# Kernel tuning notes

Measured on AMD Instinct MI355X. Metric: run time of the kernel, lower is better.

## Reference

```python
import jax, jax.numpy as jnp
from jax import lax
import numpy as np

B = 4096
CUR_OBS = 256; HIST_C = 96; HIST_T = 25
FUT_FLAT = 256 * 10  # fut_ref_dim * fut_ref_seq_len
HID = 1024; PROJ = 512; HLAT = 64; FLAT = 64
CONV = HID // 4  # conv_hidden_dim
E = 16; TOPK = 4; NGROUP = 4; TOPKG = 2; ROUTE_SCALE = 1.0; NSHARED = 2; OUT = 23

silu = jax.nn.silu

def conv1d(x, w, b, stride):
    # x: [B, C_in, T], w: [C_out, C_in, K] (torch Conv1d layout), padding=1
    y = lax.conv_general_dilated(x, w, (stride,), [(1, 1)],
                                 dimension_numbers=('NCH', 'OIH', 'NCH'))
    return y + b[None, :, None]

def setup_inputs() -> dict:
    key = jax.random.key(0)
    ks = iter(jax.random.split(key, 64))
    def nrm(shape, s=0.02):
        return jax.random.normal(next(ks), shape, jnp.float32) * s
    d = {}
    d['cur_obs'] = jax.random.normal(next(ks), (B, CUR_OBS), jnp.float32)
    d['cur_hist_seq'] = jax.random.normal(next(ks), (B, HIST_T, HIST_C), jnp.float32)
    d['fut_ref'] = jax.random.normal(next(ks), (B, FUT_FLAT), jnp.float32)
    d['vae_noise'] = jax.random.normal(next(ks), (B, FLAT), jnp.float32)
    # history conv encoder
    d['conv1_w'] = nrm((CONV, HIST_C, 3));      d['conv1_b'] = nrm((CONV,))
    d['conv2_w'] = nrm((2 * CONV, CONV, 3));    d['conv2_b'] = nrm((2 * CONV,))
    d['conv3_w'] = nrm((4 * CONV, 2 * CONV, 3)); d['conv3_b'] = nrm((4 * CONV,))
    d['hlin1_w'] = nrm((4 * CONV, HID)); d['hlin1_b'] = nrm((HID,))
    d['hlin2_w'] = nrm((HID, HLAT));     d['hlin2_b'] = nrm((HLAT,))
    # fut-ref VAE encoder
    d['enc1_w'] = nrm((FUT_FLAT, HID)); d['enc1_b'] = nrm((HID,))
    d['enc2_w'] = nrm((HID, HID));      d['enc2_b'] = nrm((HID,))
    d['enc3_w'] = nrm((HID, 2 * FLAT)); d['enc3_b'] = nrm((2 * FLAT,))
    # input projection
    d['proj_w'] = nrm((CUR_OBS + HLAT + FLAT, PROJ)); d['proj_b'] = nrm((PROJ,))
    # router
    d['router_w'] = nrm((PROJ, E)); d['router_b'] = nrm((E,))
    # stacked fine experts (DeepseekV3MLP x E)
    d['Wg'] = nrm((E, PROJ, HID)); d['bg'] = nrm((E, HID))
    d['Wu'] = nrm((E, PROJ, HID)); d['bu'] = nrm((E, HID))
    d['Wd'] = nrm((E, HID, PROJ)); d['bd'] = nrm((E, PROJ))
    # shared experts (intermediate = HID * NSHARED)
    d['sh_g_w'] = nrm((PROJ, HID * NSHARED)); d['sh_g_b'] = nrm((HID * NSHARED,))
    d['sh_u_w'] = nrm((PROJ, HID * NSHARED)); d['sh_u_b'] = nrm((HID * NSHARED,))
    d['sh_d_w'] = nrm((HID * NSHARED, PROJ)); d['sh_d_b'] = nrm((PROJ,))
    # output mlp + head
    d['out1_w'] = nrm((PROJ, HID)); d['out1_b'] = nrm((HID,))
    d['out2_w'] = nrm((HID, HID));  d['out2_b'] = nrm((HID,))
    d['head_w'] = nrm((HID, OUT));  d['head_b'] = nrm((OUT,))
    return d


def reference(cur_obs, cur_hist_seq, fut_ref, vae_noise,
              conv1_w, conv1_b, conv2_w, conv2_b, conv3_w, conv3_b,
              hlin1_w, hlin1_b, hlin2_w, hlin2_b,
              enc1_w, enc1_b, enc2_w, enc2_b, enc3_w, enc3_b,
              proj_w, proj_b, router_w, router_b,
              Wg, bg, Wu, bu, Wd, bd,
              sh_g_w, sh_g_b, sh_u_w, sh_u_b, sh_d_w, sh_d_b,
              out1_w, out1_b, out2_w, out2_b, head_w, head_b):
    # ---- history conv encoder ----
    h = cur_hist_seq.transpose(0, 2, 1)                 # [B, C, T]
    h = silu(conv1d(h, conv1_w, conv1_b, 1))            # [B, 256, 25]
    h = silu(conv1d(h, conv2_w, conv2_b, 2))            # [B, 512, 13]
    h = silu(conv1d(h, conv3_w, conv3_b, 2))            # [B, 1024, 7]
    h = h.mean(-1)                                      # AdaptiveAvgPool1d(1)+Flatten
    hist_lat = silu(h @ hlin1_w + hlin1_b) @ hlin2_w + hlin2_b  # [B, 64]
    # ---- fut-ref VAE encoder + reparameterize ----
    e = silu(fut_ref @ enc1_w + enc1_b)
    e = silu(e @ enc2_w + enc2_b)
    mu, logvar = jnp.split(e @ enc3_w + enc3_b, 2, axis=-1)
    z = mu + jnp.exp(0.5 * logvar) * vae_noise          # [B, 64]
    # ---- projection ----
    x = jnp.concatenate([cur_obs, hist_lat, z], axis=-1) @ proj_w + proj_b  # [B, PROJ]
    # ---- DeepseekV3 top-k group router (router math in fp32) ----
    logits = x.astype(jnp.float32) @ router_w + router_b
    scores = jax.nn.sigmoid(logits)                     # [B, E]
    gs = scores.reshape(-1, NGROUP, E // NGROUP)
    group_scores = lax.top_k(gs, 2)[0].sum(-1)          # [B, NGROUP]
    gidx = lax.top_k(group_scores, TOPKG)[1]
    rows = jnp.arange(scores.shape[0])[:, None]
    gmask = jnp.zeros_like(group_scores).at[rows, gidx].set(1.0)
    smask = jnp.repeat(gmask, E // NGROUP, axis=1)      # [B, E]
    masked = jnp.where(smask > 0, scores, 0.0)
    tidx = lax.top_k(masked, TOPK)[1]                   # [B, TOPK]
    tw = jnp.take_along_axis(scores, tidx, axis=1)
    tw = tw / (tw.sum(-1, keepdims=True) + 1e-20) * ROUTE_SCALE
    # ---- MoE dispatch/combine: sparse combine weights, dense expert eval ----
    w = jnp.zeros((x.shape[0], E), jnp.float32).at[rows, tidx].add(tw)  # [B, E]
    g = jnp.einsum('bh,ehi->bei', x, Wg) + bg           # [B, E, HID]
    u = jnp.einsum('bh,ehi->bei', x, Wu) + bu
    y = jnp.einsum('bei,eih->beh', silu(g) * u, Wd) + bd  # [B, E, PROJ]
    moe_out = jnp.einsum('be,beh->bh', w, y)            # [B, PROJ]
    shared = (silu(x @ sh_g_w + sh_g_b) * (x @ sh_u_w + sh_u_b)) @ sh_d_w + sh_d_b
    h2 = moe_out + shared
    h2 = silu(h2 @ out1_w + out1_b) @ out2_w + out2_b
    return h2 @ head_w + head_b                         # actions [B, OUT]
```

## Files before the change

kernel.cpp:

```cpp
#include <hip/hip_runtime.h>
#include <hip/hip_bf16.h>


#define BATCH 4096
typedef unsigned short u16;
typedef unsigned int u32;
using bf16x8 = __attribute__((ext_vector_type(8))) __bf16;
using f32x4  = __attribute__((ext_vector_type(4))) float;

__device__ __forceinline__ float silu_f(float v) { return v / (1.f + __expf(-v)); }

__device__ __forceinline__ float b2f(u16 u) {
  union { u32 i; float f; } c; c.i = ((u32)u) << 16; return c.f;
}
__device__ __forceinline__ u16 f2b(float f) {
  union { float f; u32 i; } c; c.f = f;
  u32 r = c.i + 0x7FFFu + ((c.i >> 16) & 1u);
  return (u16)(r >> 16);
}
__device__ __forceinline__ float4 ld4(const float* p) { return *(const float4*)p; }
__device__ __forceinline__ float4 ld4(const u16* p) {
  ushort4 v = *(const ushort4*)p;
  return make_float4(b2f(v.x), b2f(v.y), b2f(v.z), b2f(v.w));
}

__device__ __forceinline__ void gll16(const u16* g, u16* l) {
  __attribute__((address_space(3))) u32* lp =
      reinterpret_cast<__attribute__((address_space(3))) u32*>(
          reinterpret_cast<uintptr_t>(l));
  __builtin_amdgcn_global_load_lds(reinterpret_cast<const u32*>(g), lp, 16, 0, 0);
}

union U8 { uint4 u; bf16x8 b; };

static constexpr size_t WT1T_B = 0;
static constexpr size_t WT2T_B = 147456;
static constexpr size_t WT3T_B = 933888;
static constexpr size_t HL1T_B = 4079616;
static constexpr size_t RA_B   = 6176768;
static constexpr size_t RB_B   = 64897024;
static constexpr size_t P_B    = 119422976;
static constexpr size_t FRH_B  = RA_B;
static constexpr size_t FRL_B  = RA_B + 20971520;
static constexpr size_t E1H_B  = RA_B + 41943040;
static constexpr size_t E1L_B  = RA_B + 50331648;
static constexpr size_t E2H_B  = RA_B;
// ... 12 lines not shown
static constexpr size_t H2_B   = RA_B + 25165824;
static constexpr size_t H2B_B  = RA_B + 33554432;
static constexpr size_t E1TH_B = RB_B;
static constexpr size_t E1TL_B = RB_B + 5242880;
static constexpr size_t E2TH_B = RB_B + 10485760;
static constexpr size_t E2TL_B = RB_B + 12582912;
static constexpr size_t PENC_B = RB_B + 14680064;
static constexpr size_t HSB_B  = RB_B;
static constexpr size_t Y2_B   = RB_B;
static constexpr size_t HB_B   = RB_B;
static constexpr size_t HI1_B  = RB_B + 8388608;
static constexpr size_t PHL2_B = RB_B + 16777216;
static constexpr size_t XCH_B  = RB_B + 16777216;
static constexpr size_t XCL_B  = RB_B + 19922944;
static constexpr size_t XH_B   = RB_B;
static constexpr size_t TM_B   = RB_B + 8388608;
static constexpr size_t STB_B  = RB_B + 8388608;
static constexpr size_t PSH_B  = RB_B + 25165824;
static constexpr size_t O1B_B  = RB_B;
static constexpr size_t O2H_B  = RB_B + 16777216;
static constexpr size_t O2L_B  = RB_B + 25165824;
static constexpr size_t PHD_B  = RB_B + 33554432;
static constexpr size_t HLAT_B = P_B;
static constexpr size_t E3P_B  = P_B + 1048576;
static constexpr size_t Z_B    = P_B + 3145728;
static constexpr size_t LOG_B  = P_B + 4194304;
static constexpr size_t TID_B  = P_B + 4456448;
static constexpr size_t TW_B   = P_B + 4521984;
static constexpr size_t POS_B  = P_B + 4587520;
static constexpr size_t CNT_B  = P_B + 4653056;
static constexpr size_t OFS_B  = P_B + 4653184;
static constexpr size_t ROWL_B = P_B + 4653312;
static constexpr size_t WL_B   = P_B + 4718848;
static constexpr size_t ZP_B   = P_B + 4784384;
static constexpr size_t PRJH_B = P_B + 4788480;
static constexpr size_t PRJL_B = P_B + 5181696;
static constexpr size_t E3TH_B = P_B + 5574912;
static constexpr size_t E3TL_B = P_B + 5837056;
static constexpr size_t HL2P_B = P_B + 6099200;
static constexpr size_t HDH_B  = P_B + 6361344;
static constexpr size_t HDL_B  = P_B + 6623488;

#define TILE_DECODE(nn_)                         \
  const int bid = blockIdx.x;                    \
  const int xcd = bid & 7;                       \
  const int tt_ = bid >> 3;                      \
  const int n0 = (tt_ % (nn_)) * 128;            \
  const int m0 = ((tt_ / (nn_)) * 8 + xcd) * 128;

__global__ void k_zero2(int* __restrict__ a, int na, int* __restrict__ b, int nb) {
  int i = blockIdx.x * 256 + threadIdx.x;
  if (i < na) a[i] = 0;
  else if (i < na + nb) b[i - na] = 0;
}
__global__ void k_zero_f4(float4* __restrict__ p, int n4) {
  int i = blockIdx.x * 256 + threadIdx.x;
  if (i < n4) p[i] = make_float4(0.f, 0.f, 0.f, 0.f);
}
__global__ void k_f32_to_bf4(const float* __restrict__ s, u16* __restrict__ d, int n4) {
  int i = blockIdx.x * 256 + threadIdx.x;
  if (i >= n4) return;
  float4 v = *(const float4*)(s + (size_t)i * 4);
  *(ushort4*)(d + (size_t)i * 4) = make_ushort4(f2b(v.x), f2b(v.y), f2b(v.z), f2b(v.w));
}
__global__ void k_split_x(const float* __restrict__ s, u16* __restrict__ dh,
                          u16* __restrict__ dl, int n4) {
  int i = blockIdx.x * 256 + threadIdx.x;
  if (i >= n4) return;
  float4 v = *(const float4*)(s + (size_t)i * 4);
  float a[4] = {v.x, v.y, v.z, v.w};
  ushort4 h, l;
  u16* hp = (u16*)&h; u16* lp = (u16*)&l;
#pragma unroll
  for (int j = 0; j < 4; ++j) {
    u16 hh = f2b(a[j]);
    hp[j] = hh;
    lp[j] = f2b(a[j] - b2f(hh));
  }
  *(ushort4*)(dh + (size_t)i * 4) = h;
  *(ushort4*)(dl + (size_t)i * 4) = l;
}
// ... 2 lines not shown
                        const float* __restrict__ bias, u16* __restrict__ Ch,
                        u16* __restrict__ Cl, int N, int n4) {
  int i = blockIdx.x * 256 + threadIdx.x;
  if (i >= n4) return;
  float4 a = *(const float4*)(P0 + (size_t)i * 4);
  float4 b = *(const float4*)(P1 + (size_t)i * 4);
  int col = (i * 4) & (N - 1);
  float r[4] = {a.x + b.x, a.y + b.y, a.z + b.z, a.w + b.w};
  ushort4 h, l;
  u16* hp = (u16*)&h; u16* lp = (u16*)&l;
#pragma unroll
  for (int j = 0; j < 4; ++j) {
    float v = r[j] + bias[col + j];
    if (ACT) v = silu_f(v);
    u16 hh = f2b(v);
    hp[j] = hh;
    lp[j] = f2b(v - b2f(hh));
  }
  *(ushort4*)(Ch + (size_t)i * 4) = h;
  *(ushort4*)(Cl + (size_t)i * 4) = l;
}
template<int ACT, int EPI>
__global__ void k_combS(const float* __restrict__ P, const float* __restrict__ bias,
                        float* __restrict__ Cf, int S, int lgNp, int Nout, int total) {
  int idx = blockIdx.x * 256 + threadIdx.x;
  if (idx >= total) return;
  int row = idx >> lgNp;
  int col = idx & ((1 << lgNp) - 1);
  if (col >= Nout) return;
  float s = 0.f;
  for (int si = 0; si < S; ++si) s += P[(size_t)si * total + idx];
  s += bias[col];
  if (ACT) s = silu_f(s);
  if (EPI == 0) Cf[(size_t)row * Nout + col] = s;
  else Cf[(size_t)row * Nout + col] += s;
}
__global__ void k_concat_split(const float* __restrict__ obs,
                               const float* __restrict__ hl,
                               const float* __restrict__ z,
                               u16* __restrict__ dh, u16* __restrict__ dl) {
  int idx = blockIdx.x * 256 + threadIdx.x;
  if (idx >= BATCH * 384) return;
  int b = idx / 384, c = idx - b * 384;
  float v;
  if (c < 256)      v = obs[(size_t)b * 256 + c];
  else if (c < 320) v = hl[(size_t)b * 64 + (c - 256)];
  else              v = z[(size_t)b * 64 + (c - 320)];
  u16 h = f2b(v);
  dh[idx] = h;
  dl[idx] = f2b(v - b2f(h));
}
__global__ void k_wt_conv3(const float* __restrict__ w1, u16* __restrict__ t1,
                           const float* __restrict__ w2, u16* __restrict__ t2,
                           const float* __restrict__ w3, u16* __restrict__ t3) {
  int idx = blockIdx.x * 256 + threadIdx.x;
  const float* w; u16* t; int CIN;
  if (idx < 73728)        { w = w1; t = t1; CIN = 96; }
  else if (idx < 466944)  { idx -= 73728;  w = w2; t = t2; CIN = 256; }
  else if (idx < 2039808) { idx -= 466944; w = w3; t = t3; CIN = 512; }
  else return;
  int Kc = CIN * 3;
  int o = idx / Kc, c = idx - o * Kc;
  int k = c / CIN, i = c - k * CIN;
  t[idx] = f2b(w[(size_t)o * Kc + i * 3 + k]);
}
__global__ __launch_bounds__(256) void k_transpose_bf(const float* __restrict__ W,
                                                      u16* __restrict__ WT,
                                                      int K, int N) {
  __shared__ float t[32][33];
  int n0 = blockIdx.x * 32, k0 = blockIdx.y * 32;
  int lx = threadIdx.x & 31, ly = threadIdx.x >> 5;
#pragma unroll
  for (int r = 0; r < 32; r += 8)
    t[ly + r][lx] = W[(size_t)(k0 + ly + r) * N + n0 + lx];
  __syncthreads();
#pragma unroll
  for (int r = 0; r < 32; r += 8)
    WT[(size_t)(n0 + ly + r) * K + k0 + lx] = f2b(t[lx][ly + r]);
}
__global__ __launch_bounds__(256) void k_transpose_bf_pad(const float* __restrict__ W,
                                                          u16* __restrict__ WT,
                                                          int K, int N) {
  __shared__ float t[32][33];
  int n0 = blockIdx.x * 32, k0 = blockIdx.y * 32;
  int lx = threadIdx.x & 31, ly = threadIdx.x >> 5;
#pragma unroll
  for (int r = 0; r < 32; r += 8)
    t[ly + r][lx] = (n0 + lx < N) ? W[(size_t)(k0 + ly + r) * N + n0 + lx] : 0.f;
  __syncthreads();
#pragma unroll
  for (int r = 0; r < 32; r += 8)
    WT[(size_t)(n0 + ly + r) * K + k0 + lx] = f2b(t[lx][ly + r]);
}
__global__ __launch_bounds__(256) void k_transpose_hilo_pad(const float* __restrict__ W,
                                                            u16* __restrict__ WTh,
                                                            u16* __restrict__ WTl,
                                                            int K, int N) {
  __shared__ float t[32][33];
  int n0 = blockIdx.x * 32, k0 = blockIdx.y * 32;
  int lx = threadIdx.x & 31, ly = threadIdx.x >> 5;
#pragma unroll
  for (int r = 0; r < 32; r += 8)
    t[ly + r][lx] = (n0 + lx < N) ? W[(size_t)(k0 + ly + r) * N + n0 + lx] : 0.f;
  __syncthreads();
#pragma unroll
  for (int r = 0; r < 32; r += 8) {
    float f = t[lx][ly + r];
    u16 h = f2b(f);
    size_t o = (size_t)(n0 + ly + r) * K + k0 + lx;
    WTh[o] = h;
    WTl[o] = f2b(f - b2f(h));
  }
}
__global__ __launch_bounds__(256) void k_transpose_bf_b(const float* __restrict__ W,
                                                        u16* __restrict__ WT,
                                                        int K, int N) {
  const size_t eo = (size_t)blockIdx.z * K * N;
  __shared__ float t[32][33];
  int n0 = blockIdx.x * 32, k0 = blockIdx.y * 32;
  int lx = threadIdx.x & 31, ly = threadIdx.x >> 5;
#pragma unroll
  for (int r = 0; r < 32; r += 8)
    t[ly + r][lx] = W[eo + (size_t)(k0 + ly + r) * N + n0 + lx];
  __syncthreads();
#pragma unroll
  for (int r = 0; r < 32; r += 8)
    WT[eo + (size_t)(n0 + ly + r) * K + k0 + lx] = f2b(t[lx][ly + r]);
}
__global__ __launch_bounds__(256) void k_transpose_hilo(const float* __restrict__ W,
                                                        u16* __restrict__ WTh,
                                                        u16* __restrict__ WTl,
                                                        int K, int N) {
  __shared__ float t[32][33];
  int n0 = blockIdx.x * 32, k0 = blockIdx.y * 32;
  int lx = threadIdx.x & 31, ly = threadIdx.x >> 5;
#pragma unroll
  for (int r = 0; r < 32; r += 8)
    t[ly + r][lx] = W[(size_t)(k0 + ly + r) * N + n0 + lx];
  __syncthreads();
#pragma unroll
  for (int r = 0; r < 32; r += 8) {
    float f = t[lx][ly + r];
    u16 h = f2b(f);
    size_t o = (size_t)(n0 + ly + r) * K + k0 + lx;
    WTh[o] = h;
    WTl[o] = f2b(f - b2f(h));
  }
}

#define PRO128 \
  const int tid = threadIdx.x; \
  const int lane = tid & 63; \
  const int wid = tid >> 6; \
  const int wr = (wid >> 1) * 64, wc = (wid & 1) * 64; \
  const int l15 = lane & 15, lsub = lane >> 4;

#define MFMA_BF16(a, b, c) __builtin_amdgcn_mfma_f32_16x16x32_bf16(a, b, c, 0, 0, 0)

template<int ACT, int EPI, int AP, int BP>
__global__ __launch_bounds__(256) void k_gg(
    const u16* __restrict__ A0, const u16* __restrict__ A1,
    const u16* __restrict__ B0, const u16* __restrict__ B1,
    const float* __restrict__ bias,
    float* __restrict__ Cf, u16* __restrict__ Ch, u16* __restrict__ Cl,
    int K, int lda, int ldb, int nn, int Nout) {
  constexpr int NT = AP + BP;
  __shared__ u16 lds[NT * 4096];
  PRO128
  TILE_DECODE(nn)
  const int r0 = wid * 32 + (lane >> 2);
// ... 608 lines not shown
#pragma unroll
        for (int ni = 0; ni < 4; ++ni)
          acc[mi][ni] = MFMA_BF16(fa[mi].b, fb[ni].b, acc[mi][ni]);
    }
    __syncthreads();
  }
  const int row4 = lsub * 4;
#pragma unroll
  for (int mi = 0; mi < 4; ++mi)
#pragma unroll
    for (int j = 0; j < 4; ++j) {
      int row = m0 + wr + mi * 16 + row4 + j;
      if (row >= ne) continue;
      int r = rowlist[base + row];
      float wl = wlist[base + row];
#pragma unroll
      for (int ni = 0; ni < 4; ++ni) {
        int col = n0 + wc + ni * 16 + l15;
        atomicAdd(&h2[(size_t)r * 512 + col], wl * (acc[mi][ni][j] + bde[col]));
      }
    }
}

template<int ACT, bool NG, typename TA>
__global__ __launch_bounds__(256) void k_gemm(const TA* __restrict__ A,
                                              const float* __restrict__ W,
                                              const float* __restrict__ bias,
                                              float* __restrict__ C,
                                              int N, int K) {
  __shared__ float As[16][64];
  __shared__ float Bs[16][64];
  const int tid = threadIdx.x;
  const int m0 = blockIdx.x * 64;
  const int n0 = blockIdx.y * 64;
  const int tr = tid >> 4, tc = tid & 15;
  const int lm = tid >> 2, lk = (tid & 3) * 4;
  const int ln = tid & 63, lkb = (tid >> 6) * 4;
  float acc[4][4] = {};
  for (int k0 = 0; k0 < K; k0 += 16) {
    float4 av = ld4(A + (size_t)(m0 + lm) * K + k0 + lk);
    As[lk + 0][lm] = av.x; As[lk + 1][lm] = av.y;
    As[lk + 2][lm] = av.z; As[lk + 3][lm] = av.w;
#pragma unroll
    for (int s = 0; s < 4; ++s) {
      int kk = lkb + s;
      float v = 0.f;
      if (!NG || (n0 + ln) < N) v = W[(size_t)(k0 + kk) * N + n0 + ln];
      Bs[kk][ln] = v;
    }
    __syncthreads();
#pragma unroll
    for (int kk = 0; kk < 16; ++kk) {
      float4 a4 = *(const float4*)&As[kk][tr * 4];
      float4 b4 = *(const float4*)&Bs[kk][tc * 4];
      float a[4] = {a4.x, a4.y, a4.z, a4.w};
      float b[4] = {b4.x, b4.y, b4.z, b4.w};
#pragma unroll
      for (int i = 0; i < 4; ++i)
#pragma unroll
        for (int j = 0; j < 4; ++j) acc[i][j] = fmaf(a[i], b[j], acc[i][j]);
    }
    __syncthreads();
  }
#pragma unroll
  for (int i = 0; i < 4; ++i) {
    int m = m0 + tr * 4 + i;
#pragma unroll
    for (int j = 0; j < 4; ++j) {
      int n = n0 + tc * 4 + j;
      if (NG && n >= N) continue;
      float v = acc[i][j] + bias[n];
      if (ACT == 1) v = silu_f(v);
      C[(size_t)m * N + n] = v;
    }
  }
}

__global__ void k_mean7(const u16* __restrict__ y3, u16* __restrict__ hb) {
  int idx = blockIdx.x * 256 + threadIdx.x;
  if (idx >= BATCH * 1024) return;
  int b = idx >> 10, o = idx & 1023;
  const u16* p = y3 + (size_t)b * 7 * 1024 + o;
  float s = 0.f;
#pragma unroll
  for (int t = 0; t < 7; ++t) s += b2f(p[(size_t)t * 1024]);
  hb[idx] = f2b(s * (1.f / 7.f));
}

__global__ void k_z(const float* __restrict__ e3, const float* __restrict__ noise,
                    float* __restrict__ z) {
  int idx = blockIdx.x * 256 + threadIdx.x;
  if (idx >= BATCH * 64) return;
  int b = idx >> 6, j = idx & 63;
  float mu = e3[(size_t)b * 128 + j];
  float lv = e3[(size_t)b * 128 + 64 + j];
  z[idx] = mu + expf(0.5f * lv) * noise[idx];
}

__global__ void k_router(const float* __restrict__ logits, int* __restrict__ tidA,
                         float* __restrict__ twA, int* __restrict__ posA,
                         int* __restrict__ counts) {
  int b = blockIdx.x * 256 + threadIdx.x;
  if (b >= BATCH) return;
  float s[16];
#pragma unroll
  for (int e = 0; e < 16; ++e)
    s[e] = 1.f / (1.f + expf(-logits[(size_t)b * 16 + e]));
  float gsc[4];
#pragma unroll
  for (int g = 0; g < 4; ++g) {
    float m1 = -1e30f; int i1 = -1;
    for (int i = 0; i < 4; ++i) { float v = s[g * 4 + i]; if (v > m1) { m1 = v; i1 = i; } }
    float m2 = -1e30f;
    for (int i = 0; i < 4; ++i) { if (i == i1) continue; float v = s[g * 4 + i]; if (v > m2) m2 = v; }
    gsc[g] = m1 + m2;
  }
  int g1 = 0; float b1 = gsc[0];
  for (int g = 1; g < 4; ++g) if (gsc[g] > b1) { b1 = gsc[g]; g1 = g; }
  int g2 = -1; float b2 = -1e30f;
// ... 12 lines not shown
      if (!used[e] && ms[e] > best) { best = ms[e]; bi = e; }
    used[bi] = true;
    te[t] = bi;
    tv[t] = s[bi];
    tsum += s[bi];
  }
  float inv = 1.f / (tsum + 1e-20f);
  for (int t = 0; t < 4; ++t) {
    int e = te[t];
    tidA[b * 4 + t] = e;
    twA[b * 4 + t] = tv[t] * inv;
    posA[b * 4 + t] = atomicAdd(&counts[e], 1);
  }
}

__global__ void k_offsets(const int* __restrict__ counts, int* __restrict__ offs) {
  if (threadIdx.x == 0 && blockIdx.x == 0) {
    int a = 0;
    for (int e = 0; e < 16; ++e) { offs[e] = a; a += counts[e]; }
    offs[16] = a;
  }
}

__global__ void k_build(const int* __restrict__ tidA, const float* __restrict__ twA,
                        const int* __restrict__ posA, const int* __restrict__ offs,
                        int* __restrict__ rowlist, float* __restrict__ wlist) {
  int idx = blockIdx.x * 256 + threadIdx.x;
  if (idx >= BATCH * 4) return;
  int e = tidA[idx];
  int p = offs[e] + posA[idx];
  rowlist[p] = idx >> 2;
  wlist[p] = twA[idx];
}

extern "C" void kernel_launch(void* const* d_in, const int* in_sizes, int n_in,
                              void* d_out, int out_size, void* d_ws, size_t ws_size,
                              hipStream_t stream) {
  const float* cur_obs  = (const float*)d_in[0];
  const float* hist_seq = (const float*)d_in[1];
  const float* fut_ref  = (const float*)d_in[2];
  const float* noise    = (const float*)d_in[3];
  const float* conv1_w  = (const float*)d_in[4];
  const float* conv1_b  = (const float*)d_in[5];
  const float* conv2_w  = (const float*)d_in[6];
  const float* conv2_b  = (const float*)d_in[7];
  const float* conv3_w  = (const float*)d_in[8];
  const float* conv3_b  = (const float*)d_in[9];
  const float* hlin1_w  = (const float*)d_in[10];
  const float* hlin1_b  = (const float*)d_in[11];
  const float* hlin2_w  = (const float*)d_in[12];
  const float* hlin2_b  = (const float*)d_in[13];
  const float* enc1_w   = (const float*)d_in[14];
  const float* enc1_b   = (const float*)d_in[15];
  const float* enc2_w   = (const float*)d_in[16];
  const float* enc2_b   = (const float*)d_in[17];
// ... 48 lines not shown
  u16* o2T   = (u16*)(wsb + O2T_B);
  float* h2  = (float*)(wsb + H2_B);
  u16* h2b   = (u16*)(wsb + H2B_B);
  u16* e1Th  = (u16*)(wsb + E1TH_B);
  u16* e1Tl  = (u16*)(wsb + E1TL_B);
  u16* e2Th  = (u16*)(wsb + E2TH_B);
  u16* e2Tl  = (u16*)(wsb + E2TL_B);
  float* Penc = (float*)(wsb + PENC_B);
  float* Phl2 = (float*)(wsb + PHL2_B);
  float* Psh  = (float*)(wsb + PSH_B);
  float* Phd  = (float*)(wsb + PHD_B);
  u16* hsb   = (u16*)(wsb + HSB_B);
  u16* hb    = (u16*)(wsb + HB_B);
  u16* hi1b  = (u16*)(wsb + HI1_B);
  u16* xch   = (u16*)(wsb + XCH_B);
  u16* xcl   = (u16*)(wsb + XCL_B);
  u16* xh    = (u16*)(wsb + XH_B);
  u16* tmoeb = (u16*)(wsb + TM_B);
  u16* stb   = (u16*)(wsb + STB_B);
  u16* o1b   = (u16*)(wsb + O1B_B);
  u16* o2h   = (u16*)(wsb + O2H_B);
  u16* o2l   = (u16*)(wsb + O2L_B);
  float* hlat = (float*)(wsb + HLAT_B);
  float* e3   = (float*)(wsb + E3P_B);
  float* z    = (float*)(wsb + Z_B);
  float* logitsb = (float*)(wsb + LOG_B);
  int*   tidA  = (int*)(wsb + TID_B);
  float* twA   = (float*)(wsb + TW_B);
  int*   posA  = (int*)(wsb + POS_B);
  int*   counts = (int*)(wsb + CNT_B);
  int*   offs  = (int*)(wsb + OFS_B);
  int*   rowlist = (int*)(wsb + ROWL_B);
  float* wlist = (float*)(wsb + WL_B);
  u16*   zp    = (u16*)(wsb + ZP_B);
  u16* prjTh = (u16*)(wsb + PRJH_B);
  u16* prjTl = (u16*)(wsb + PRJL_B);
  u16* e3Th  = (u16*)(wsb + E3TH_B);
  u16* e3Tl  = (u16*)(wsb + E3TL_B);
  u16* hl2P  = (u16*)(wsb + HL2P_B);
  u16* hdTh  = (u16*)(wsb + HDH_B);
  u16* hdTl  = (u16*)(wsb + HDL_B);

  k_zero2<<<dim3(5), 256, 0, stream>>>(counts, 16, (int*)zp, 1024);

  k_wt_conv3<<<dim3(7968), 256, 0, stream>>>(conv1_w, wt1T, conv2_w, wt2T, conv3_w, wt3T);
  k_transpose_bf<<<dim3(32, 32), 256, 0, stream>>>(hlin1_w, hl1T, 1024, 1024);
  k_transpose_hilo<<<dim3(32, 80), 256, 0, stream>>>(enc1_w, e1Th, e1Tl, 2560, 1024);
  k_transpose_hilo<<<dim3(32, 32), 256, 0, stream>>>(enc2_w, e2Th, e2Tl, 1024, 1024);
  k_transpose_hilo<<<dim3(4, 32), 256, 0, stream>>>(enc3_w, e3Th, e3Tl, 1024, 128);
  k_transpose_hilo<<<dim3(16, 12), 256, 0, stream>>>(proj_w, prjTh, prjTl, 384, 512);
  k_transpose_bf_pad<<<dim3(4, 32), 256, 0, stream>>>(hlin2_w, hl2P, 1024, 64);
  k_transpose_hilo_pad<<<dim3(4, 32), 256, 0, stream>>>(head_w, hdTh, hdTl, 1024, 23);

  k_split_x<<<dim3(10240), 256, 0, stream>>>(fut_ref, frh, frl, BATCH * 2560 / 4);
  k_ggps<2, 2><<<dim3(512), 256, 0, stream>>>(frh, frl, e1Th, e1Tl, Penc,
                                              1280, 2560, 2560, 8, 1024, 256);
  k_comb2<1><<<dim3(4096), 256, 0, stream>>>(Penc, Penc + (size_t)BATCH * 1024,
                                             enc1_b, e1h, e1l, 1024, BATCH * 1024 / 4);
  k_ggps<2, 2><<<dim3(512), 256, 0, stream>>>(e1h, e1l, e2Th, e2Tl, Penc,
                                              512, 1024, 1024, 8, 1024, 256);
  k_comb2<1><<<dim3(4096), 256, 0, stream>>>(Penc, Penc + (size_t)BATCH * 1024,
                                             enc2_b, e2h, e2l, 1024, BATCH * 1024 / 4);
  k_ggps<2, 2><<<dim3(128), 256, 0, stream>>>(e2h, e2l, e3Th, e3Tl, Penc,
                                              256, 1024, 1024, 1, 128, 32);
  k_combS<0, 0><<<dim3(2048), 256, 0, stream>>>(Penc, enc3_b, e3, 4, 7, 128, BATCH * 128);
  k_z<<<dim3(1024), 256, 0, stream>>>(e3, noise, z);

  k_f32_to_bf4<<<dim3(9600), 256, 0, stream>>>(hist_seq, hsb, BATCH * 25 * 96 / 4);
  k_gconv32<96, 25, 25, 1><<<dim3(1600), 256, 0, stream>>>(hsb, wt1T, conv1_b, y1b, zp, 256, 2);
  k_gconv64<256, 25, 13, 2><<<dim3(1664), 256, 0, stream>>>(y1b, wt2T, conv2_b, y2b, zp, 512, 4);
  k_gconv64<512, 13, 7, 2><<<dim3(1792), 256, 0, stream>>>(y2b, wt3T, conv3_b, y3b, zp, 1024, 8);
  k_mean7<<<dim3(16384), 256, 0, stream>>>(y3b, hb);
  k_gg64<1, 1><<<dim3(256), 256, 0, stream>>>(hb, hl1T, hlin1_b,
      nullptr, hi1b, nullptr, 1024, 1024, 1024, 8, 1024);
  k_ggps<1, 1><<<dim3(128), 256, 0, stream>>>(hi1b, nullptr, hl2P, nullptr, Phl2,
                                              256, 1024, 1024, 1, 128, 32);
  k_combS<0, 0><<<dim3(2048), 256, 0, stream>>>(Phl2, hlin2_b, hlat, 4, 7, 64, BATCH * 128);

  k_transpose_bf_b<<<dim3(32, 16, 16), 256, 0, stream>>>(Wg, wgT, 512, 1024);
  k_transpose_bf_b<<<dim3(32, 16, 16), 256, 0, stream>>>(Wu, wuT, 512, 1024);
  k_transpose_bf_b<<<dim3(16, 32, 16), 256, 0, stream>>>(Wd, wdT, 1024, 512);

  k_concat_split<<<dim3(6144), 256, 0, stream>>>(cur_obs, hlat, z, xch, xcl);
  k_gg<0, 0, 2, 2><<<dim3(128), 256, 0, stream>>>(xch, xcl, prjTh, prjTl, proj_b,
      x, nullptr, nullptr, 384, 384, 384, 4, 512);
  k_gemm<0, true, float><<<dim3(64, 1), 256, 0, stream>>>(x, router_w, router_b, logitsb, 16, 512);
  k_router<<<dim3(16), 256, 0, stream>>>(logitsb, tidA, twA, posA, counts);
  k_offsets<<<dim3(1), 64, 0, stream>>>(counts, offs);
  k_build<<<dim3(64), 256, 0, stream>>>(tidA, twA, posA, offs, rowlist, wlist);
  k_f32_to_bf4<<<dim3(2048), 256, 0, stream>>>(x, xh, BATCH * 512 / 4);

  k_gmoeup<<<dim3(4096), 256, 0, stream>>>(xh, wgT, wuT, bg, bu,
                                           rowlist, counts, offs, zp, tmoeb);

  k_transpose_bf<<<dim3(64, 16), 256, 0, stream>>>(shg_w, shgT, 512, 2048);
  k_transpose_bf<<<dim3(64, 16), 256, 0, stream>>>(shu_w, shuT, 512, 2048);
  k_transpose_bf<<<dim3(16, 64), 256, 0, stream>>>(shd_w, shdT, 2048, 512);
  k_transpose_bf<<<dim3(32, 16), 256, 0, stream>>>(out1_w, o1T, 512, 1024);
  k_transpose_bf<<<dim3(32, 32), 256, 0, stream>>>(out2_w, o2T, 1024, 1024);
  k_zero_f4<<<dim3(2048), 256, 0, stream>>>((float4*)h2, BATCH * 512 / 4);

  k_gmoedown64<<<dim3(2048), 256, 0, stream>>>(tmoeb, wdT, bd, rowlist, wlist,
                                               counts, offs, zp, h2);

  k_gdual1<<<dim3(512), 256, 0, stream>>>(xh, shgT, shuT, shg_b, shu_b,
                                          stb, 2048, 512, 512, 512, 16);
  k_ggps<1, 1><<<dim3(256), 256, 0, stream>>>(stb, nullptr, shdT, nullptr, Psh,
                                              1024, 2048, 2048, 4, 512, 128);
  k_combS<0, 2><<<dim3(8192), 256, 0, stream>>>(Psh, shd_b, h2, 2, 9, 512, BATCH * 512);

  k_f32_to_bf4<<<dim3(2048), 256, 0, stream>>>(h2, h2b, BATCH * 512 / 4);
  k_gg64<1, 1><<<dim3(256), 256, 0, stream>>>(h2b, o1T, out1_b,
      nullptr, o1b, nullptr, 512, 512, 512, 8, 1024);
  k_gg64<0, 3><<<dim3(256), 256, 0, stream>>>(o1b, o2T, out2_b,
      nullptr, o2h, o2l, 1024, 1024, 1024, 8, 1024);
  k_ggps<2, 2><<<dim3(128), 256, 0, stream>>>(o2h, o2l, hdTh, hdTl, Phd,
                                              256, 1024, 1024, 1, 128, 32);
  k_combS<0, 0><<<dim3(2048), 256, 0, stream>>>(Phd, head_b, (float*)d_out, 4, 7, 23, BATCH * 128);
}
```

Before: 991.4 us.

## Merge weight-prep launches, fuse small epilogues, and replace router GEMM

Collapses the many weight transpose/convert and zeroing launches into three grouped prep kernels, cutting launch count and tail gaps. It also fuses the bf16 conversion of x into the routing list builder, and fuses the h2 bf16 cast into the shared-expert combine. The VAE z sampling is fused into the split-K reduction, and several narrow split-K GEMMs now use smaller K chunks with twice the partials. The tiny 16-wide router GEMM becomes a dedicated per-row kernel with LDS-resident weights. More partial slices raise reduction traffic slightly, and the large fused prep kernels branch on block index.

```diff
diff --git a/kernel.cpp b/kernel.cpp
--- a/kernel.cpp
+++ b/kernel.cpp
@@ -17,11 +17,6 @@
   union { float f; u32 i; } c; c.f = f;
   u32 r = c.i + 0x7FFFu + ((c.i >> 16) & 1u);
   return (u16)(r >> 16);
-}
-__device__ __forceinline__ float4 ld4(const float* p) { return *(const float4*)p; }
-__device__ __forceinline__ float4 ld4(const u16* p) {
-  ushort4 v = *(const ushort4*)p;
-  return make_float4(b2f(v.x), b2f(v.y), b2f(v.z), b2f(v.w));
 }
 
 __device__ __forceinline__ void gll16(const u16* g, u16* l) {
@@ -80,7 +75,6 @@
 static constexpr size_t O2L_B  = RB_B + 25165824;
 static constexpr size_t PHD_B  = RB_B + 33554432;
 static constexpr size_t HLAT_B = P_B;
-static constexpr size_t E3P_B  = P_B + 1048576;
 static constexpr size_t Z_B    = P_B + 3145728;
 static constexpr size_t LOG_B  = P_B + 4194304;
 static constexpr size_t TID_B  = P_B + 4456448;
@@ -106,15 +100,141 @@
   const int n0 = (tt_ % (nn_)) * 128;            \
   const int m0 = ((tt_ / (nn_)) * 8 + xcd) * 128;
 
-__global__ void k_zero2(int* __restrict__ a, int na, int* __restrict__ b, int nb) {
-  int i = blockIdx.x * 256 + threadIdx.x;
-  if (i < na) a[i] = 0;
-  else if (i < na + nb) b[i - na] = 0;
-}
-__global__ void k_zero_f4(float4* __restrict__ p, int n4) {
-  int i = blockIdx.x * 256 + threadIdx.x;
-  if (i < n4) p[i] = make_float4(0.f, 0.f, 0.f, 0.f);
-}
+__device__ __forceinline__ void dev_tr_bf(const float* __restrict__ W, u16* __restrict__ WT,
+                                          int K, int N, int Ng, int n0, int k0,
+                                          int tid, float (*t)[33]) {
+  int lx = tid & 31, ly = tid >> 5;
+#pragma unroll
+  for (int r = 0; r < 32; r += 8)
+    t[ly + r][lx] = (n0 + lx < Ng) ? W[(size_t)(k0 + ly + r) * N + n0 + lx] : 0.f;
+  __syncthreads();
+#pragma unroll
+  for (int r = 0; r < 32; r += 8)
+    WT[(size_t)(n0 + ly + r) * K + k0 + lx] = f2b(t[lx][ly + r]);
+}
+__device__ __forceinline__ void dev_tr_hilo(const float* __restrict__ W, u16* __restrict__ WTh,
+                                            u16* __restrict__ WTl, int K, int N, int Ng,
+                                            int n0, int k0, int tid, float (*t)[33]) {
+  int lx = tid & 31, ly = tid >> 5;
+#pragma unroll
+  for (int r = 0; r < 32; r += 8)
+    t[ly + r][lx] = (n0 + lx < Ng) ? W[(size_t)(k0 + ly + r) * N + n0 + lx] : 0.f;
+  __syncthreads();
+#pragma unroll
+  for (int r = 0; r < 32; r += 8) {
+    float f = t[lx][ly + r];
+    u16 h = f2b(f);
+    size_t o = (size_t)(n0 + ly + r) * K + k0 + lx;
+    WTh[o] = h;
+    WTl[o] = f2b(f - b2f(h));
+  }
+}
+
+__global__ __launch_bounds__(256) void k_prep_w(
+    int* __restrict__ counts, int* __restrict__ zpi,
+    const float* __restrict__ c1w, u16* __restrict__ wt1T,
+    const float* __restrict__ c2w, u16* __restrict__ wt2T,
+    const float* __restrict__ c3w, u16* __restrict__ wt3T,
+    const float* __restrict__ hlin1_w, u16* __restrict__ hl1T,
+    const float* __restrict__ enc1_w, u16* __restrict__ e1Th, u16* __restrict__ e1Tl,
+    const float* __restrict__ enc2_w, u16* __restrict__ e2Th, u16* __restrict__ e2Tl,
+    const float* __restrict__ enc3_w, u16* __restrict__ e3Th, u16* __restrict__ e3Tl,
+    const float* __restrict__ proj_w, u16* __restrict__ prjTh, u16* __restrict__ prjTl,
+    const float* __restrict__ head_w, u16* __restrict__ hdTh, u16* __restrict__ hdTl,
+    const float* __restrict__ hlin2_w, u16* __restrict__ hl2P) {
+  __shared__ float t[32][33];
+  int b = blockIdx.x;
+  const int tid = threadIdx.x;
+  if (b < 5) {
+    int i = b * 256 + tid;
+    if (i < 16) counts[i] = 0;
+    else if (i < 1040) zpi[i - 16] = 0;
+    return;
+  }
+  b -= 5;
+  if (b < 7968) {
+    int idx = b * 256 + tid;
+    const float* w; u16* tt; int CIN;
+    if (idx < 73728)        { w = c1w; tt = wt1T; CIN = 96; }
+    else if (idx < 466944)  { idx -= 73728;  w = c2w; tt = wt2T; CIN = 256; }
+    else if (idx < 2039808) { idx -= 466944; w = c3w; tt = wt3T; CIN = 512; }
+    else return;
+    int Kc = CIN * 3;
+    int o = idx / Kc, c = idx - o * Kc;
+    int k = c / CIN, i = c - k * CIN;
+    tt[idx] = f2b(w[(size_t)o * Kc + i * 3 + k]);
+    return;
+  }
+  b -= 7968;
+  if (b < 1024) { dev_tr_bf(hlin1_w, hl1T, 1024, 1024, 1024, (b & 31) * 32, (b >> 5) * 32, tid, t); return; }
+  b -= 1024;
+  if (b < 2560) { dev_tr_hilo(enc1_w, e1Th, e1Tl, 2560, 1024, 1024, (b & 31) * 32, (b >> 5) * 32, tid, t); return; }
+  b -= 2560;
+  if (b < 1024) { dev_tr_hilo(enc2_w, e2Th, e2Tl, 1024, 1024, 1024, (b & 31) * 32, (b >> 5) * 32, tid, t); return; }
+  b -= 1024;
+  if (b < 128) { dev_tr_hilo(enc3_w, e3Th, e3Tl, 1024, 128, 128, (b & 3) * 32, (b >> 2) * 32, tid, t); return; }
+  b -= 128;
+  if (b < 192) { dev_tr_hilo(proj_w, prjTh, prjTl, 384, 512, 512, (b & 15) * 32, (b >> 4) * 32, tid, t); return; }
+  b -= 192;
+  if (b < 128) { dev_tr_hilo(head_w, hdTh, hdTl, 1024, 23, 23, (b & 3) * 32, (b >> 2) * 32, tid, t); return; }
+  b -= 128;
+  dev_tr_bf(hlin2_w, hl2P, 1024, 64, 64, (b & 3) * 32, (b >> 2) * 32, tid, t);
+}
+
+__global__ __launch_bounds__(256) void k_prep_exp(
+    const float* __restrict__ Wg, u16* __restrict__ wgT,
+    const float* __restrict__ Wu, u16* __restrict__ wuT,
+    const float* __restrict__ Wd, u16* __restrict__ wdT) {
+  __shared__ float t[32][33];
+  int b = blockIdx.x;
+  const int tid = threadIdx.x;
+  if (b < 8192) {
+    int e = b >> 9, r = b & 511;
+    dev_tr_bf(Wg + (size_t)e * 512 * 1024, wgT + (size_t)e * 512 * 1024,
+              512, 1024, 1024, (r & 31) * 32, (r >> 5) * 32, tid, t);
+    return;
+  }
+  b -= 8192;
+  if (b < 8192) {
+    int e = b >> 9, r = b & 511;
+    dev_tr_bf(Wu + (size_t)e * 512 * 1024, wuT + (size_t)e * 512 * 1024,
+              512, 1024, 1024, (r & 31) * 32, (r >> 5) * 32, tid, t);
+    return;
+  }
+  b -= 8192;
+  {
+    int e = b >> 9, r = b & 511;
+    dev_tr_bf(Wd + (size_t)e * 1024 * 512, wdT + (size_t)e * 1024 * 512,
+              1024, 512, 512, (r & 15) * 32, (r >> 4) * 32, tid, t);
+  }
+}
+
+__global__ __launch_bounds__(256) void k_prep_post(
+    const float* __restrict__ shg_w, u16* __restrict__ shgT,
+    const float* __restrict__ shu_w, u16* __restrict__ shuT,
+    const float* __restrict__ shd_w, u16* __restrict__ shdT,
+    const float* __restrict__ o1w, u16* __restrict__ o1T,
+    const float* __restrict__ o2w, u16* __restrict__ o2T,
+    float4* __restrict__ h2z) {
+  __shared__ float t[32][33];
+  int b = blockIdx.x;
+  const int tid = threadIdx.x;
+  if (b < 1024) { dev_tr_bf(shg_w, shgT, 512, 2048, 2048, (b & 63) * 32, (b >> 6) * 32, tid, t); return; }
+  b -= 1024;
+  if (b < 1024) { dev_tr_bf(shu_w, shuT, 512, 2048, 2048, (b & 63) * 32, (b >> 6) * 32, tid, t); return; }
+  b -= 1024;
+  if (b < 1024) { dev_tr_bf(shd_w, shdT, 2048, 512, 512, (b & 15) * 32, (b >> 4) * 32, tid, t); return; }
+  b -= 1024;
+  if (b < 512) { dev_tr_bf(o1w, o1T, 512, 1024, 1024, (b & 31) * 32, (b >> 5) * 32, tid, t); return; }
+  b -= 512;
+  if (b < 1024) { dev_tr_bf(o2w, o2T, 1024, 1024, 1024, (b & 31) * 32, (b >> 5) * 32, tid, t); return; }
+  b -= 1024;
+  {
+    int i = b * 256 + tid;
+    if (i < BATCH * 512 / 4) h2z[i] = make_float4(0.f, 0.f, 0.f, 0.f);
+  }
+}
+
 __global__ void k_f32_to_bf4(const float* __restrict__ s, u16* __restrict__ d, int n4) {
   int i = blockIdx.x * 256 + threadIdx.x;
   if (i >= n4) return;
@@ -163,7 +283,8 @@
 }
 template<int ACT, int EPI>
 __global__ void k_combS(const float* __restrict__ P, const float* __restrict__ bias,
-                        float* __restrict__ Cf, int S, int lgNp, int Nout, int total) {
+                        float* __restrict__ Cf, u16* __restrict__ Ch,
+                        int S, int lgNp, int Nout, int total) {
   int idx = blockIdx.x * 256 + threadIdx.x;
   if (idx >= total) return;
   int row = idx >> lgNp;
@@ -174,7 +295,24 @@
   s += bias[col];
   if (ACT) s = silu_f(s);
   if (EPI == 0) Cf[(size_t)row * Nout + col] = s;
-  else Cf[(size_t)row * Nout + col] += s;
+  else if (EPI == 2) Cf[(size_t)row * Nout + col] += s;
+  else {
+    s += Cf[(size_t)row * Nout + col];
+    Ch[(size_t)row * Nout + col] = f2b(s);
+  }
+}
+__global__ void k_combz(const float* __restrict__ P, const float* __restrict__ eb,
+                        const float* __restrict__ noise, float* __restrict__ z, int S) {
+  int idx = blockIdx.x * 256 + threadIdx.x;
+  if (idx >= BATCH * 64) return;
+  int b = idx >> 6, j = idx & 63;
+  float mu = eb[j], lv = eb[64 + j];
+  for (int si = 0; si < S; ++si) {
+    const float* Pk = P + (size_t)si * BATCH * 128 + (size_t)b * 128;
+    mu += Pk[j];
+    lv += Pk[64 + j];
+  }
+  z[idx] = mu + expf(0.5f * lv) * noise[idx];
 }
 __global__ void k_concat_split(const float* __restrict__ obs,
                                const float* __restrict__ hl,
@@ -190,103 +328,6 @@
   u16 h = f2b(v);
   dh[idx] = h;
   dl[idx] = f2b(v - b2f(h));
-}
-__global__ void k_wt_conv3(const float* __restrict__ w1, u16* __restrict__ t1,
-                           const float* __restrict__ w2, u16* __restrict__ t2,
-                           const float* __restrict__ w3, u16* __restrict__ t3) {
-  int idx = blockIdx.x * 256 + threadIdx.x;
-  const float* w; u16* t; int CIN;
-  if (idx < 73728)        { w = w1; t = t1; CIN = 96; }
-  else if (idx < 466944)  { idx -= 73728;  w = w2; t = t2; CIN = 256; }
-  else if (idx < 2039808) { idx -= 466944; w = w3; t = t3; CIN = 512; }
-  else return;
-  int Kc = CIN * 3;
-  int o = idx / Kc, c = idx - o * Kc;
-  int k = c / CIN, i = c - k * CIN;
-  t[idx] = f2b(w[(size_t)o * Kc + i * 3 + k]);
-}
-__global__ __launch_bounds__(256) void k_transpose_bf(const float* __restrict__ W,
-                                                      u16* __restrict__ WT,
-                                                      int K, int N) {
-  __shared__ float t[32][33];
-  int n0 = blockIdx.x * 32, k0 = blockIdx.y * 32;
-  int lx = threadIdx.x & 31, ly = threadIdx.x >> 5;
-#pragma unroll
-  for (int r = 0; r < 32; r += 8)
-    t[ly + r][lx] = W[(size_t)(k0 + ly + r) * N + n0 + lx];
-  __syncthreads();
-#pragma unroll
-  for (int r = 0; r < 32; r += 8)
-    WT[(size_t)(n0 + ly + r) * K + k0 + lx] = f2b(t[lx][ly + r]);
-}
-__global__ __launch_bounds__(256) void k_transpose_bf_pad(const float* __restrict__ W,
-                                                          u16* __restrict__ WT,
-                                                          int K, int N) {
-  __shared__ float t[32][33];
-  int n0 = blockIdx.x * 32, k0 = blockIdx.y * 32;
-  int lx = threadIdx.x & 31, ly = threadIdx.x >> 5;
-#pragma unroll
-  for (int r = 0; r < 32; r += 8)
-    t[ly + r][lx] = (n0 + lx < N) ? W[(size_t)(k0 + ly + r) * N + n0 + lx] : 0.f;
-  __syncthreads();
-#pragma unroll
-  for (int r = 0; r < 32; r += 8)
-    WT[(size_t)(n0 + ly + r) * K + k0 + lx] = f2b(t[lx][ly + r]);
-}
-__global__ __launch_bounds__(256) void k_transpose_hilo_pad(const float* __restrict__ W,
-                                                            u16* __restrict__ WTh,
-                                                            u16* __restrict__ WTl,
-                                                            int K, int N) {
-  __shared__ float t[32][33];
-  int n0 = blockIdx.x * 32, k0 = blockIdx.y * 32;
-  int lx = threadIdx.x & 31, ly = threadIdx.x >> 5;
-#pragma unroll
-  for (int r = 0; r < 32; r += 8)
-    t[ly + r][lx] = (n0 + lx < N) ? W[(size_t)(k0 + ly + r) * N + n0 + lx] : 0.f;
-  __syncthreads();
-#pragma unroll
-  for (int r = 0; r < 32; r += 8) {
-    float f = t[lx][ly + r];
-    u16 h = f2b(f);
-    size_t o = (size_t)(n0 + ly + r) * K + k0 + lx;
-    WTh[o] = h;
-    WTl[o] = f2b(f - b2f(h));
-  }
-}
-__global__ __launch_bounds__(256) void k_transpose_bf_b(const float* __restrict__ W,
-                                                        u16* __restrict__ WT,
-                                                        int K, int N) {
-  const size_t eo = (size_t)blockIdx.z * K * N;
-  __shared__ float t[32][33];
-  int n0 = blockIdx.x * 32, k0 = blockIdx.y * 32;
-  int lx = threadIdx.x & 31, ly = threadIdx.x >> 5;
-#pragma unroll
-  for (int r = 0; r < 32; r += 8)
-    t[ly + r][lx] = W[eo + (size_t)(k0 + ly + r) * N + n0 + lx];
-  __syncthreads();
-#pragma unroll
-  for (int r = 0; r < 32; r += 8)
-    WT[eo + (size_t)(n0 + ly + r) * K + k0 + lx] = f2b(t[lx][ly + r]);
-}
-__global__ __launch_bounds__(256) void k_transpose_hilo(const float* __restrict__ W,
-                                                        u16* __restrict__ WTh,
-                                                        u16* __restrict__ WTl,
-                                                        int K, int N) {
-  __shared__ float t[32][33];
-  int n0 = blockIdx.x * 32, k0 = blockIdx.y * 32;
-  int lx = threadIdx.x & 31, ly = threadIdx.x >> 5;
-#pragma unroll
-  for (int r = 0; r < 32; r += 8)
-    t[ly + r][lx] = W[(size_t)(k0 + ly + r) * N + n0 + lx];
-  __syncthreads();
-#pragma unroll
-  for (int r = 0; r < 32; r += 8) {
-    float f = t[lx][ly + r];
-    u16 h = f2b(f);
-    size_t o = (size_t)(n0 + ly + r) * K + k0 + lx;
-    WTh[o] = h;
-    WTl[o] = f2b(f - b2f(h));
-  }
 }
 
 #define PRO128 \
@@ -941,57 +982,38 @@
     }
 }
 
-template<int ACT, bool NG, typename TA>
-__global__ __launch_bounds__(256) void k_gemm(const TA* __restrict__ A,
-                                              const float* __restrict__ W,
-                                              const float* __restrict__ bias,
-                                              float* __restrict__ C,
-                                              int N, int K) {
-  __shared__ float As[16][64];
-  __shared__ float Bs[16][64];
+__global__ __launch_bounds__(256) void k_logits(const float* __restrict__ x,
+                                                const float* __restrict__ W,
+                                                const float* __restrict__ bias,
+                                                float* __restrict__ out) {
+  __shared__ float Ws[512 * 17];
   const int tid = threadIdx.x;
-  const int m0 = blockIdx.x * 64;
-  const int n0 = blockIdx.y * 64;
-  const int tr = tid >> 4, tc = tid & 15;
-  const int lm = tid >> 2, lk = (tid & 3) * 4;
-  const int ln = tid & 63, lkb = (tid >> 6) * 4;
-  float acc[4][4] = {};
-  for (int k0 = 0; k0 < K; k0 += 16) {
-    float4 av = ld4(A + (size_t)(m0 + lm) * K + k0 + lk);
-    As[lk + 0][lm] = av.x; As[lk + 1][lm] = av.y;
-    As[lk + 2][lm] = av.z; As[lk + 3][lm] = av.w;
-#pragma unroll
-    for (int s = 0; s < 4; ++s) {
-      int kk = lkb + s;
-      float v = 0.f;
-      if (!NG || (n0 + ln) < N) v = W[(size_t)(k0 + kk) * N + n0 + ln];
-      Bs[kk][ln] = v;
-    }
-    __syncthreads();
-#pragma unroll
-    for (int kk = 0; kk < 16; ++kk) {
-      float4 a4 = *(const float4*)&As[kk][tr * 4];
-      float4 b4 = *(const float4*)&Bs[kk][tc * 4];
-      float a[4] = {a4.x, a4.y, a4.z, a4.w};
-      float b[4] = {b4.x, b4.y, b4.z, b4.w};
-#pragma unroll
-      for (int i = 0; i < 4; ++i)
-#pragma unroll
-        for (int j = 0; j < 4; ++j) acc[i][j] = fmaf(a[i], b[j], acc[i][j]);
-    }
-    __syncthreads();
-  }
-#pragma unroll
-  for (int i = 0; i < 4; ++i) {
-    int m = m0 + tr * 4 + i;
-#pragma unroll
-    for (int j = 0; j < 4; ++j) {
-      int n = n0 + tc * 4 + j;
-      if (NG && n >= N) continue;
-      float v = acc[i][j] + bias[n];
-      if (ACT == 1) v = silu_f(v);
-      C[(size_t)m * N + n] = v;
-    }
+  for (int i = tid; i < 8192; i += 256) {
+    int k = i >> 4, e = i & 15;
+    Ws[k * 17 + e] = W[i];
+  }
+  __syncthreads();
+  const int rowg = tid >> 5, l32 = tid & 31;
+  const int row = blockIdx.x * 8 + rowg;
+  const float* xr = x + (size_t)row * 512;
+  float acc[16];
+#pragma unroll
+  for (int e = 0; e < 16; ++e) acc[e] = 0.f;
+#pragma unroll
+  for (int kb = 0; kb < 16; ++kb) {
+    int k = l32 + 32 * kb;
+    float xv = xr[k];
+    const float* wr = Ws + k * 17;
+#pragma unroll
+    for (int e = 0; e < 16; ++e) acc[e] = fmaf(xv, wr[e], acc[e]);
+  }
+#pragma unroll
+  for (int m = 1; m < 32; m <<= 1)
+#pragma unroll
+    for (int e = 0; e < 16; ++e) acc[e] += __shfl_xor(acc[e], m, 64);
+  if (l32 == 0) {
+#pragma unroll
+    for (int e = 0; e < 16; ++e) out[(size_t)row * 16 + e] = acc[e] + bias[e];
   }
 }
 
@@ -1004,16 +1026,6 @@
 #pragma unroll
   for (int t = 0; t < 7; ++t) s += b2f(p[(size_t)t * 1024]);
   hb[idx] = f2b(s * (1.f / 7.f));
-}
-
-__global__ void k_z(const float* __restrict__ e3, const float* __restrict__ noise,
-                    float* __restrict__ z) {
-  int idx = blockIdx.x * 256 + threadIdx.x;
-  if (idx >= BATCH * 64) return;
-  int b = idx >> 6, j = idx & 63;
-  float mu = e3[(size_t)b * 128 + j];
-  float lv = e3[(size_t)b * 128 + 64 + j];
-  z[idx] = mu + expf(0.5f * lv) * noise[idx];
 }
 
 __global__ void k_router(const float* __restrict__ logits, int* __restrict__ tidA,
@@ -1072,15 +1084,22 @@
   }
 }
 
-__global__ void k_build(const int* __restrict__ tidA, const float* __restrict__ twA,
-                        const int* __restrict__ posA, const int* __restrict__ offs,
-                        int* __restrict__ rowlist, float* __restrict__ wlist) {
+__global__ void k_build_bf(const int* __restrict__ tidA, const float* __restrict__ twA,
+                           const int* __restrict__ posA, const int* __restrict__ offs,
+                           int* __restrict__ rowlist, float* __restrict__ wlist,
+                           const float* __restrict__ x, u16* __restrict__ xh) {
   int idx = blockIdx.x * 256 + threadIdx.x;
-  if (idx >= BATCH * 4) return;
-  int e = tidA[idx];
-  int p = offs[e] + posA[idx];
-  rowlist[p] = idx >> 2;
-  wlist[p] = twA[idx];
+  if (idx < BATCH * 4) {
+    int e = tidA[idx];
+    int p = offs[e] + posA[idx];
+    rowlist[p] = idx >> 2;
+    wlist[p] = twA[idx];
+    return;
+  }
+  int j = idx - BATCH * 4;
+  if (j >= BATCH * 512 / 4) return;
+  float4 v = *(const float4*)(x + (size_t)j * 4);
+  *(ushort4*)(xh + (size_t)j * 4) = make_ushort4(f2b(v.x), f2b(v.y), f2b(v.z), f2b(v.w));
 }
 
 extern "C" void kernel_launch(void* const* d_in, const int* in_sizes, int n_in,
@@ -1175,7 +1194,6 @@
   u16* o2h   = (u16*)(wsb + O2H_B);
   u16* o2l   = (u16*)(wsb + O2L_B);
   float* hlat = (float*)(wsb + HLAT_B);
-  float* e3   = (float*)(wsb + E3P_B);
   float* z    = (float*)(wsb + Z_B);
   float* logitsb = (float*)(wsb + LOG_B);
   int*   tidA  = (int*)(wsb + TID_B);
@@ -1194,16 +1212,12 @@
   u16* hdTh  = (u16*)(wsb + HDH_B);
   u16* hdTl  = (u16*)(wsb + HDL_B);
 
-  k_zero2<<<dim3(5), 256, 0, stream>>>(counts, 16, (int*)zp, 1024);
-
-  k_wt_conv3<<<dim3(7968), 256, 0, stream>>>(conv1_w, wt1T, conv2_w, wt2T, conv3_w, wt3T);
-  k_transpose_bf<<<dim3(32, 32), 256, 0, stream>>>(hlin1_w, hl1T, 1024, 1024);
-  k_transpose_hilo<<<dim3(32, 80), 256, 0, stream>>>(enc1_w, e1Th, e1Tl, 2560, 1024);
-  k_transpose_hilo<<<dim3(32, 32), 256, 0, stream>>>(enc2_w, e2Th, e2Tl, 1024, 1024);
-  k_transpose_hilo<<<dim3(4, 32), 256, 0, stream>>>(enc3_w, e3Th, e3Tl, 1024, 128);
-  k_transpose_hilo<<<dim3(16, 12), 256, 0, stream>>>(proj_w, prjTh, prjTl, 384, 512);
-  k_transpose_bf_pad<<<dim3(4, 32), 256, 0, stream>>>(hlin2_w, hl2P, 1024, 64);
-  k_transpose_hilo_pad<<<dim3(4, 32), 256, 0, stream>>>(head_w, hdTh, hdTl, 1024, 23);
+  k_prep_w<<<dim3(13157), 256, 0, stream>>>(
+      counts, (int*)zp,
+      conv1_w, wt1T, conv2_w, wt2T, conv3_w, wt3T,
+      hlin1_w, hl1T,
+      enc1_w, e1Th, e1Tl, enc2_w, e2Th, e2Tl, enc3_w, e3Th, e3Tl,
+      proj_w, prjTh, prjTl, head_w, hdTh, hdTl, hlin2_w, hl2P);
 
   k_split_x<<<dim3(10240), 256, 0, stream>>>(fut_ref, frh, frl, BATCH * 2560 / 4);
   k_ggps<2, 2><<<dim3(512), 256, 0, stream>>>(frh, frl, e1Th, e1Tl, Penc,
@@ -1214,10 +1228,9 @@
                                               512, 1024, 1024, 8, 1024, 256);
   k_comb2<1><<<dim3(4096), 256, 0, stream>>>(Penc, Penc + (size_t)BATCH * 1024,
                                              enc2_b, e2h, e2l, 1024, BATCH * 1024 / 4);
-  k_ggps<2, 2><<<dim3(128), 256, 0, stream>>>(e2h, e2l, e3Th, e3Tl, Penc,
-                                              256, 1024, 1024, 1, 128, 32);
-  k_combS<0, 0><<<dim3(2048), 256, 0, stream>>>(Penc, enc3_b, e3, 4, 7, 128, BATCH * 128);
-  k_z<<<dim3(1024), 256, 0, stream>>>(e3, noise, z);
+  k_ggps<2, 2><<<dim3(256), 256, 0, stream>>>(e2h, e2l, e3Th, e3Tl, Penc,
+                                              128, 1024, 1024, 1, 128, 32);
+  k_combz<<<dim3(1024), 256, 0, stream>>>(Penc, enc3_b, noise, z, 8);
 
   k_f32_to_bf4<<<dim3(9600), 256, 0, stream>>>(hist_seq, hsb, BATCH * 25 * 96 / 4);
   k_gconv32<96, 25, 25, 1><<<dim3(1600), 256, 0, stream>>>(hsb, wt1T, conv1_b, y1b, zp, 256, 2);
@@ -1226,32 +1239,26 @@
   k_mean7<<<dim3(16384), 256, 0, stream>>>(y3b, hb);
   k_gg64<1, 1><<<dim3(256), 256, 0, stream>>>(hb, hl1T, hlin1_b,
       nullptr, hi1b, nullptr, 1024, 1024, 1024, 8, 1024);
-  k_ggps<1, 1><<<dim3(128), 256, 0, stream>>>(hi1b, nullptr, hl2P, nullptr, Phl2,
-                                              256, 1024, 1024, 1, 128, 32);
-  k_combS<0, 0><<<dim3(2048), 256, 0, stream>>>(Phl2, hlin2_b, hlat, 4, 7, 64, BATCH * 128);
-
-  k_transpose_bf_b<<<dim3(32, 16, 16), 256, 0, stream>>>(Wg, wgT, 512, 1024);
-  k_transpose_bf_b<<<dim3(32, 16, 16), 256, 0, stream>>>(Wu, wuT, 512, 1024);
-  k_transpose_bf_b<<<dim3(16, 32, 16), 256, 0, stream>>>(Wd, wdT, 1024, 512);
+  k_ggps<1, 1><<<dim3(256), 256, 0, stream>>>(hi1b, nullptr, hl2P, nullptr, Phl2,
+                                              128, 1024, 1024, 1, 128, 32);
+  k_combS<0, 0><<<dim3(2048), 256, 0, stream>>>(Phl2, hlin2_b, hlat, nullptr,
+                                                8, 7, 64, BATCH * 128);
+
+  k_prep_exp<<<dim3(24576), 256, 0, stream>>>(Wg, wgT, Wu, wuT, Wd, wdT);
 
   k_concat_split<<<dim3(6144), 256, 0, stream>>>(cur_obs, hlat, z, xch, xcl);
   k_gg<0, 0, 2, 2><<<dim3(128), 256, 0, stream>>>(xch, xcl, prjTh, prjTl, proj_b,
       x, nullptr, nullptr, 384, 384, 384, 4, 512);
-  k_gemm<0, true, float><<<dim3(64, 1), 256, 0, stream>>>(x, router_w, router_b, logitsb, 16, 512);
+  k_logits<<<dim3(512), 256, 0, stream>>>(x, router_w, router_b, logitsb);
   k_router<<<dim3(16), 256, 0, stream>>>(logitsb, tidA, twA, posA, counts);
   k_offsets<<<dim3(1), 64, 0, stream>>>(counts, offs);
-  k_build<<<dim3(64), 256, 0, stream>>>(tidA, twA, posA, offs, rowlist, wlist);
-  k_f32_to_bf4<<<dim3(2048), 256, 0, stream>>>(x, xh, BATCH * 512 / 4);
+  k_build_bf<<<dim3(2112), 256, 0, stream>>>(tidA, twA, posA, offs, rowlist, wlist, x, xh);
 
   k_gmoeup<<<dim3(4096), 256, 0, stream>>>(xh, wgT, wuT, bg, bu,
                                            rowlist, counts, offs, zp, tmoeb);
 
-  k_transpose_bf<<<dim3(64, 16), 256, 0, stream>>>(shg_w, shgT, 512, 2048);
-  k_transpose_bf<<<dim3(64, 16), 256, 0, stream>>>(shu_w, shuT, 512, 2048);
-  k_transpose_bf<<<dim3(16, 64), 256, 0, stream>>>(shd_w, shdT, 2048, 512);
-  k_transpose_bf<<<dim3(32, 16), 256, 0, stream>>>(out1_w, o1T, 512, 1024);
-  k_transpose_bf<<<dim3(32, 32), 256, 0, stream>>>(out2_w, o2T, 1024, 1024);
-  k_zero_f4<<<dim3(2048), 256, 0, stream>>>((float4*)h2, BATCH * 512 / 4);
+  k_prep_post<<<dim3(6656), 256, 0, stream>>>(shg_w, shgT, shu_w, shuT, shd_w, shdT,
+                                              out1_w, o1T, out2_w, o2T, (float4*)h2);
 
   k_gmoedown64<<<dim3(2048), 256, 0, stream>>>(tmoeb, wdT, bd, rowlist, wlist,
                                                counts, offs, zp, h2);
@@ -1260,14 +1267,15 @@
                                           stb, 2048, 512, 512, 512, 16);
   k_ggps<1, 1><<<dim3(256), 256, 0, stream>>>(stb, nullptr, shdT, nullptr, Psh,
                                               1024, 2048, 2048, 4, 512, 128);
-  k_combS<0, 2><<<dim3(8192), 256, 0, stream>>>(Psh, shd_b, h2, 2, 9, 512, BATCH * 512);
-
-  k_f32_to_bf4<<<dim3(2048), 256, 0, stream>>>(h2, h2b, BATCH * 512 / 4);
+  k_combS<0, 3><<<dim3(8192), 256, 0, stream>>>(Psh, shd_b, h2, h2b,
+                                                2, 9, 512, BATCH * 512);
+
   k_gg64<1, 1><<<dim3(256), 256, 0, stream>>>(h2b, o1T, out1_b,
       nullptr, o1b, nullptr, 512, 512, 512, 8, 1024);
   k_gg64<0, 3><<<dim3(256), 256, 0, stream>>>(o1b, o2T, out2_b,
       nullptr, o2h, o2l, 1024, 1024, 1024, 8, 1024);
-  k_ggps<2, 2><<<dim3(128), 256, 0, stream>>>(o2h, o2l, hdTh, hdTl, Phd,
-                                              256, 1024, 1024, 1, 128, 32);
-  k_combS<0, 0><<<dim3(2048), 256, 0, stream>>>(Phd, head_b, (float*)d_out, 4, 7, 23, BATCH * 128);
-}
+  k_ggps<2, 2><<<dim3(256), 256, 0, stream>>>(o2h, o2l, hdTh, hdTl, Phd,
+                                              128, 1024, 1024, 1, 128, 32);
+  k_combS<0, 0><<<dim3(2048), 256, 0, stream>>>(Phd, head_b, (float*)d_out, nullptr,
+                                                8, 7, 23, BATCH * 128);
+}
```

Measured after the change: 905.7 us (median of 2 runs). 1.09x faster.
